# Optimization experiments

Hardware: AMD Instinct MI355X
Metric: run time of the kernel (lower is better)

Reference implementation:

```python
import jax, jax.numpy as jnp
import numpy as np

N_SRC = 100_000
N_DST = 100_000
N_EDGES = 1_600_000
D_IN = 256
N_HEADS = 4
OUT_FEATS = 32
NEG_SLOPE = 0.2


def setup_inputs() -> dict:
    key = jax.random.key(0)
    k1, k2, k3, k4, k5, k6, k7 = jax.random.split(key, 7)
    return {
        "feat_src": jax.random.normal(k1, (N_SRC, D_IN), dtype=jnp.float32),
        "feat_dst": jax.random.normal(k2, (N_DST, D_IN), dtype=jnp.float32),
        "w_src": jax.random.normal(k3, (D_IN, N_HEADS * OUT_FEATS), dtype=jnp.float32) * 0.05,
        "w_dst": jax.random.normal(k4, (D_IN, N_HEADS * OUT_FEATS), dtype=jnp.float32) * 0.05,
        "attn": jax.random.normal(k5, (N_HEADS, 2 * OUT_FEATS), dtype=jnp.float32) * 0.05,
        "src_idx": jax.random.randint(k6, (N_EDGES,), 0, N_SRC, dtype=jnp.int32),
        "dst_idx": jax.random.randint(k7, (N_EDGES,), 0, N_DST, dtype=jnp.int32),
    }


def reference(feat_src, feat_dst, w_src, w_dst, attn, src_idx, dst_idx):
    H, two_d = attn.shape
    D = two_d // 2
    n_dst = feat_dst.shape[0]
    # node transformations (dropout rate = 0.0 -> identity)
    fs = (feat_src @ w_src).reshape(-1, H, D)   # [Ns, H, D]
    fd = (feat_dst @ w_dst).reshape(-1, H, D)   # [Nd, H, D]
    # per-node attention logits: e_dst uses first half, e_src second half
    e_dst = (fd * attn[:, :D]).sum(-1)          # [Nd, H]
    e_src = (fs * attn[:, D:]).sum(-1)          # [Ns, H]
    # u_add_v on edges + leaky relu
    e = e_src[src_idx] + e_dst[dst_idx]         # [E, H]
    e = jnp.where(e > 0, e, NEG_SLOPE * e)
    # edge softmax: segment softmax over incoming edges of each dst node
    m = jax.ops.segment_max(e, dst_idx, num_segments=n_dst)       # [Nd, H]
    m = jnp.where(jnp.isfinite(m), m, 0.0)                        # empty segments
    ex = jnp.exp(e - m[dst_idx])                                  # [E, H]
    denom = jax.ops.segment_sum(ex, dst_idx, num_segments=n_dst)  # [Nd, H]
    a = ex / denom[dst_idx]                                       # [E, H]
    # u_mul_e + sum aggregation
    msg = fs[src_idx] * a[:, :, None]                             # [E, H, D]
    out = jax.ops.segment_sum(msg, dst_idx, num_segments=n_dst)   # [Nd, H, D]
    return jax.nn.relu(out.reshape(n_dst, H * D))
```

## Files before the change

### kernel.cpp

```cpp
#include <hip/hip_runtime.h>

#define N_NODES 100000
#define N_EDGES 1600000
#define D_IN    256
#define HD      128
#define NEG_SLOPE 0.2f

#define BUK_SH    5
#define BUK_NODES 32
#define NBUCKETS ((N_NODES + BUK_NODES - 1) / BUK_NODES)
#define BUK_CAP  1024
#define BUK_CH   8192
#define NB_BUK   ((N_EDGES + BUK_CH - 1) / BUK_CH)

#define NB_GEMM ((N_NODES + 255) / 256)
#define NB_EDST 256
#define NB_PREP 33

#define EX_STRIDE 1032

typedef __bf16 bf16x8 __attribute__((ext_vector_type(8)));
typedef float  f32x4  __attribute__((ext_vector_type(4)));

__device__ __forceinline__ float lrelu_exp(float v) {
  v = v > 0.f ? v : NEG_SLOPE * v;
  return __expf(v);
}
__device__ __forceinline__ float bf_lo(unsigned u) { return __uint_as_float(u << 16); }
__device__ __forceinline__ float bf_hi(unsigned u) { return __uint_as_float(u & 0xffff0000u); }

__global__ __launch_bounds__(1024) void prep_bucket_kernel(const float* __restrict__ w_src,
                                                           const float* __restrict__ w_dst,
                                                           const float* __restrict__ attn,
                                                           ushort* __restrict__ wT,
                                                           float* __restrict__ v_dst,
                                                           const int* __restrict__ src,
                                                           const int* __restrict__ dstv,
                                                           int* __restrict__ bcur,
                                                           unsigned* __restrict__ ebuk) {
  const int bid = blockIdx.x;
  const int tid = threadIdx.x;
  if (bid < 32) {
    int idx = bid * 1024 + tid;
    int k = idx >> 7, n = idx & 127;
    __bf16 bv = (__bf16)w_src[idx];
    wT[n * 256 + k] = *(const ushort*)&bv;
  } else if (bid == 32) {
    if (tid < 256) {
      int k = tid;
      for (int h = 0; h < 4; ++h) {
        float s = 0.f;
        for (int d = 0; d < 32; ++d)
          s += w_dst[k * HD + h * 32 + d] * attn[h * 64 + d];
        v_dst[k * 4 + h] = s;
      }
    }
  } else {
    __shared__ int bh[NBUCKETS];
    const int e0 = (bid - NB_PREP) * BUK_CH;
    for (int j = tid; j < NBUCKETS; j += 1024) bh[j] = 0;
    __syncthreads();
    for (int i = tid; i < BUK_CH; i += 1024) {
      int e = e0 + i;
      if (e < N_EDGES) atomicAdd(&bh[dstv[e] >> BUK_SH], 1);
    }
    __syncthreads();
    for (int j = tid; j < NBUCKETS; j += 1024) {
      int c = bh[j];
      bh[j] = (c > 0) ? atomicAdd(&bcur[j], c) : 0;
    }
    __syncthreads();
    for (int i = tid; i < BUK_CH; i += 1024) {
      int e = e0 + i;
      if (e < N_EDGES) {
        int d = dstv[e];
        int b = d >> BUK_SH;
        int p = atomicAdd(&bh[b], 1);
        if (p < BUK_CAP)
          ebuk[(size_t)b * BUK_CAP + p] =
              ((unsigned)src[e] << BUK_SH) | (unsigned)(d & (BUK_NODES - 1));
      }
    }
  }
}

__global__ __launch_bounds__(1024) void gemm_edst_kernel(const float* __restrict__ A,
                                                         const ushort* __restrict__ wT16,
                                                         const float* __restrict__ attn,
                                                         unsigned* __restrict__ fs16,
                                                         float* __restrict__ e_src,
                                                         const float* __restrict__ feat_dst,
                                                         const float* __restrict__ v_dst,
                                                         float* __restrict__ e_dst,
                                                         int M) {
  __shared__ ushort Bl[128 * 256];
  const int bid = blockIdx.x;
  const int tid = threadIdx.x;
  const int lane = tid & 63, wid = tid >> 6;
  const int lr = lane & 15, hi = lane >> 4;

  if (bid < NB_GEMM) {
    {
      const uint4* wg4 = (const uint4*)wT16;
#pragma unroll
      for (int i = 0; i < 4; ++i) {
        int c = i * 1024 + tid;
        int col = c >> 5;
        unsigned byte = ((unsigned)c * 16u) ^ (((unsigned)col & 31u) << 4);
        *(uint4*)((char*)Bl + byte) = wg4[c];
      }
    }

    f32x4 acc[8];
    const f32x4 zf = {0.f, 0.f, 0.f, 0.f};
#pragma unroll
    for (int n = 0; n < 8; ++n) acc[n] = zf;

    const int bm = bid * 256;
    int row0 = bm + wid * 16 + lr;
    int row0c = row0 < M ? row0 : M - 1;
    const float* a0p = A + (size_t)row0c * D_IN;

    __syncthreads();

#pragma unroll
    for (int ks = 0; ks < 8; ++ks) {
      const int ko = ks * 32 + hi * 8;
      float4 u0 = *(const float4*)(a0p + ko);
      float4 u1 = *(const float4*)(a0p + ko + 4);
      bf16x8 af0;
      af0[0] = (__bf16)u0.x; af0[1] = (__bf16)u0.y; af0[2] = (__bf16)u0.z; af0[3] = (__bf16)u0.w;
      af0[4] = (__bf16)u1.x; af0[5] = (__bf16)u1.y; af0[6] = (__bf16)u1.z; af0[7] = (__bf16)u1.w;
      bf16x8 bf[8];
#pragma unroll
      for (int n = 0; n < 8; ++n) {
        unsigned col = (unsigned)(n * 16 + lr);
        unsigned byte = (col * 512u + (unsigned)(ks * 64 + hi * 16)) ^ ((col & 31u) << 4);
        bf[n] = *(const bf16x8*)((const char*)Bl + byte);
      }
#pragma unroll
      for (int n = 0; n < 8; ++n)
        acc[n] = __builtin_amdgcn_mfma_f32_16x16x32_bf16(af0, bf[n], acc[n], 0, 0, 0);
    }

#pragma unroll
    for (int n = 0; n < 8; ++n) {
#pragma unroll
      for (int r4 = 0; r4 < 4; ++r4) {
        float val = acc[n][r4];
        float pv  = __shfl_xor(val, 1, 64);
        int gr = bm + wid * 16 + hi * 4 + r4;
        if (!(lane & 1) && gr < M) {
          __bf16 b0 = (__bf16)val, b1 = (__bf16)pv;
          unsigned pk = ((unsigned)*(const ushort*)&b1 << 16) | *(const ushort*)&b0;
          fs16[(size_t)gr * 64 + n * 8 + (lr >> 1)] = pk;
        }
      }
    }

#pragma unroll
    for (int gh = 0; gh < 4; ++gh) {
      float av0 = attn[gh * 64 + 32 + lr];
      float av1 = attn[gh * 64 + 48 + lr];
#pragma unroll
      for (int r4 = 0; r4 < 4; ++r4) {
        float s = acc[2 * gh][r4] * av0 + acc[2 * gh + 1][r4] * av1;
        s += __shfl_xor(s, 1, 64);
        s += __shfl_xor(s, 2, 64);
        s += __shfl_xor(s, 4, 64);
        s += __shfl_xor(s, 8, 64);
        int gr = bm + wid * 16 + hi * 4 + r4;
        if (lr == 0 && gr < M) e_src[(size_t)gr * 4 + gh] = s;
      }
    }
  } else {
    float4* vds = (float4*)Bl;
    if (tid < 256) vds[tid] = ((const float4*)v_dst)[tid];
    __syncthreads();
    const int l = tid & 15;
    const int grp = tid >> 4;
    for (int n = (bid - NB_GEMM) * 64 + grp; n < N_NODES; n += NB_EDST * 64) {
      const float* fp = feat_dst + (size_t)n * D_IN;
      float ax = 0.f, ay = 0.f, az = 0.f, aw = 0.f;
#pragma unroll
      for (int c = 0; c < 4; ++c) {
        const int k0 = c * 64 + l * 4;
        float4 f = *(const float4*)(fp + k0);
        float4 v0 = vds[k0 + 0], v1 = vds[k0 + 1], v2 = vds[k0 + 2], v3 = vds[k0 + 3];
        ax = fmaf(f.x, v0.x, fmaf(f.y, v1.x, fmaf(f.z, v2.x, fmaf(f.w, v3.x, ax))));
        ay = fmaf(f.x, v0.y, fmaf(f.y, v1.y, fmaf(f.z, v2.y, fmaf(f.w, v3.y, ay))));
        az = fmaf(f.x, v0.z, fmaf(f.y, v1.z, fmaf(f.z, v2.z, fmaf(f.w, v3.z, az))));
        aw = fmaf(f.x, v0.w, fmaf(f.y, v1.w, fmaf(f.z, v2.w, fmaf(f.w, v3.w, aw))));
      }
#pragma unroll
      for (int off = 1; off < 16; off <<= 1) {
        ax += __shfl_xor(ax, off, 64);
        ay += __shfl_xor(ay, off, 64);
        az += __shfl_xor(az, off, 64);
        aw += __shfl_xor(aw, off, 64);
      }
      if (l == 0) *(float4*)(e_dst + (size_t)n * 4) = make_float4(ax, ay, az, aw);
    }
  }
}

__global__ __launch_bounds__(256) void agg_kernel(const unsigned* __restrict__ ebuk,
                                                  const int* __restrict__ bcur,
                                                  const float4* __restrict__ e_src,
                                                  const float4* __restrict__ e_dst,
                                                  const unsigned* __restrict__ fs16,
                                                  float* __restrict__ out, int N) {
  __shared__ unsigned sorted_e[BUK_CAP];
  __shared__ float ex_s[4][EX_STRIDE];
  __shared__ int lcnt[BUK_NODES];
  __shared__ int lofs_s[BUK_NODES + 1];
  __shared__ int lcur[BUK_NODES];
  const int tid = threadIdx.x;
  const int wslot = tid >> 6;
  const int lane = tid & 63;
  const int lo = blockIdx.x * BUK_NODES;
  const size_t start = (size_t)blockIdx.x * BUK_CAP;
  const int cnt_e = min(bcur[blockIdx.x], BUK_CAP);

  if (tid < BUK_NODES) lcnt[tid] = 0;
  __syncthreads();
  for (int i = tid; i < cnt_e; i += 256)
    atomicAdd(&lcnt[ebuk[start + i] & (BUK_NODES - 1)], 1);
  __syncthreads();
  if (tid == 0) {
    int run = 0;
    for (int j = 0; j < BUK_NODES; ++j) {
      lofs_s[j] = run; lcur[j] = run; run += lcnt[j];
    }
    lofs_s[BUK_NODES] = run;
  }
  __syncthreads();
  for (int i = tid; i < cnt_e; i += 256) {
    unsigned e = ebuk[start + i];
    int p = atomicAdd(&lcur[e & (BUK_NODES - 1)], 1);
    sorted_e[p] = e;
  }
  __syncthreads();

  for (int i = tid; i < cnt_e; i += 256) {
    unsigned ent = sorted_e[i];
    int s  = (int)(ent >> BUK_SH);
    int dl = (int)(ent & (BUK_NODES - 1));
    float4 a  = e_src[s];
    float4 ed = e_dst[lo + dl];
    ex_s[0][i] = lrelu_exp(a.x + ed.x);
    ex_s[1][i] = lrelu_exp(a.y + ed.y);
    ex_s[2][i] = lrelu_exp(a.z + ed.z);
    ex_s[3][i] = lrelu_exp(a.w + ed.w);
  }
  __syncthreads();

  const int g = lane >> 4;
  const int q = lane & 15;
  const int h = q >> 2;

  for (int nl = wslot * 8; nl < wslot * 8 + 8; ++nl) {
    int node = lo + nl;
    if (node >= N) break;
    const int nb = lofs_s[nl], ne = lofs_s[nl + 1];
    float a0=0.f,a1=0.f,a2=0.f,a3=0.f,a4=0.f,a5=0.f,a6=0.f,a7=0.f,den=0.f;

    for (int cb = nb; cb < ne; cb += 16) {
      int e0 = cb + g, e1 = e0 + 4, e2 = e0 + 8, e3 = e0 + 12;
      bool p0 = e0 < ne, p1 = e1 < ne, p2 = e2 < ne, p3 = e3 < ne;
      int c0 = p0 ? e0 : nb, c1 = p1 ? e1 : nb, c2 = p2 ? e2 : nb, c3 = p3 ? e3 : nb;
      int s0 = (int)(sorted_e[c0] >> BUK_SH);
      int s1 = (int)(sorted_e[c1] >> BUK_SH);
      int s2 = (int)(sorted_e[c2] >> BUK_SH);
      int s3 = (int)(sorted_e[c3] >> BUK_SH);
      uint4 u0 = *(const uint4*)(fs16 + (size_t)s0 * 64 + q * 4);
      uint4 u1 = *(const uint4*)(fs16 + (size_t)s1 * 64 + q * 4);
      uint4 u2 = *(const uint4*)(fs16 + (size_t)s2 * 64 + q * 4);
      uint4 u3 = *(const uint4*)(fs16 + (size_t)s3 * 64 + q * 4);
      float x0 = p0 ? ex_s[h][c0] : 0.f;
      float x1 = p1 ? ex_s[h][c1] : 0.f;
      float x2 = p2 ? ex_s[h][c2] : 0.f;
      float x3 = p3 ? ex_s[h][c3] : 0.f;
      a0 = fmaf(x0, bf_lo(u0.x), a0); a1 = fmaf(x0, bf_hi(u0.x), a1);
      a2 = fmaf(x0, bf_lo(u0.y), a2); a3 = fmaf(x0, bf_hi(u0.y), a3);
      a4 = fmaf(x0, bf_lo(u0.z), a4); a5 = fmaf(x0, bf_hi(u0.z), a5);
      a6 = fmaf(x0, bf_lo(u0.w), a6); a7 = fmaf(x0, bf_hi(u0.w), a7);
      a0 = fmaf(x1, bf_lo(u1.x), a0); a1 = fmaf(x1, bf_hi(u1.x), a1);
      a2 = fmaf(x1, bf_lo(u1.y), a2); a3 = fmaf(x1, bf_hi(u1.y), a3);
      a4 = fmaf(x1, bf_lo(u1.z), a4); a5 = fmaf(x1, bf_hi(u1.z), a5);
      a6 = fmaf(x1, bf_lo(u1.w), a6); a7 = fmaf(x1, bf_hi(u1.w), a7);
      a0 = fmaf(x2, bf_lo(u2.x), a0); a1 = fmaf(x2, bf_hi(u2.x), a1);
      a2 = fmaf(x2, bf_lo(u2.y), a2); a3 = fmaf(x2, bf_hi(u2.y), a3);
      a4 = fmaf(x2, bf_lo(u2.z), a4); a5 = fmaf(x2, bf_hi(u2.z), a5);
      a6 = fmaf(x2, bf_lo(u2.w), a6); a7 = fmaf(x2, bf_hi(u2.w), a7);
      a0 = fmaf(x3, bf_lo(u3.x), a0); a1 = fmaf(x3, bf_hi(u3.x), a1);
      a2 = fmaf(x3, bf_lo(u3.y), a2); a3 = fmaf(x3, bf_hi(u3.y), a3);
      a4 = fmaf(x3, bf_lo(u3.z), a4); a5 = fmaf(x3, bf_hi(u3.z), a5);
      a6 = fmaf(x3, bf_lo(u3.w), a6); a7 = fmaf(x3, bf_hi(u3.w), a7);
      den += x0 + x1 + x2 + x3;
    }

    den += __shfl_xor(den, 16, 64); den += __shfl_xor(den, 32, 64);
    a0 += __shfl_xor(a0, 16, 64); a0 += __shfl_xor(a0, 32, 64);
    a1 += __shfl_xor(a1, 16, 64); a1 += __shfl_xor(a1, 32, 64);
    a2 += __shfl_xor(a2, 16, 64); a2 += __shfl_xor(a2, 32, 64);
    a3 += __shfl_xor(a3, 16, 64); a3 += __shfl_xor(a3, 32, 64);
    a4 += __shfl_xor(a4, 16, 64); a4 += __shfl_xor(a4, 32, 64);
    a5 += __shfl_xor(a5, 16, 64); a5 += __shfl_xor(a5, 32, 64);
    a6 += __shfl_xor(a6, 16, 64); a6 += __shfl_xor(a6, 32, 64);
    a7 += __shfl_xor(a7, 16, 64); a7 += __shfl_xor(a7, 32, 64);
    if (lane < 16) {
      float inv = den > 0.f ? 1.f / den : 0.f;
      float4 o1, o2;
      o1.x = fmaxf(a0 * inv, 0.f); o1.y = fmaxf(a1 * inv, 0.f);
      o1.z = fmaxf(a2 * inv, 0.f); o1.w = fmaxf(a3 * inv, 0.f);
      o2.x = fmaxf(a4 * inv, 0.f); o2.y = fmaxf(a5 * inv, 0.f);
      o2.z = fmaxf(a6 * inv, 0.f); o2.w = fmaxf(a7 * inv, 0.f);
      float* op = out + (size_t)node * HD + q * 8;
      *(float4*)(op)     = o1;
      *(float4*)(op + 4) = o2;
    }
  }
}

extern "C" void kernel_launch(void* const* d_in, const int* in_sizes, int n_in,
                              void* d_out, int out_size, void* d_ws, size_t ws_size,
                              hipStream_t stream) {
  const float* feat_src = (const float*)d_in[0];
  const float* feat_dst = (const float*)d_in[1];
  const float* w_src    = (const float*)d_in[2];
  const float* w_dst    = (const float*)d_in[3];
  const float* attn     = (const float*)d_in[4];
  const int*   src_idx  = (const int*)d_in[5];
  const int*   dst_idx  = (const int*)d_in[6];
  float* out = (float*)d_out;
  char* ws = (char*)d_ws;

  unsigned* fs16  = (unsigned*)(ws);
  float*    e_src = (float*)(ws + 25600000);
  float*    e_dst = (float*)(ws + 27200000);
  unsigned* ebuk  = (unsigned*)(ws + 28800000);
  float*    v_dst = (float*)(ws + 41600000);
  ushort*   wT16  = (ushort*)(ws + 41604096);
  int*      bcur  = (int*)  (ws + 41669632);

  hipMemsetAsync(bcur, 0, NBUCKETS * sizeof(int), stream);

  prep_bucket_kernel<<<NB_PREP + NB_BUK, 1024, 0, stream>>>(
      w_src, w_dst, attn, wT16, v_dst, src_idx, dst_idx, bcur, ebuk);

  gemm_edst_kernel<<<NB_GEMM + NB_EDST, 1024, 0, stream>>>(
      feat_src, wT16, attn, fs16, e_src, feat_dst, v_dst, e_dst, N_NODES);

  agg_kernel<<<NBUCKETS, 256, 0, stream>>>(ebuk, bcur,
      (const float4*)e_src, (const float4*)e_dst, fs16, out, N_NODES);
}
```

Baseline: 164.9 us.

## Split GEMM and e_dst into separate kernels with smaller blocks and prefetched A rows

Splits the fused GEMM/e_dst kernel into a dedicated MFMA GEMM kernel (512 threads, 128 rows per block, launch bounds allowing 4 blocks per CU) and a separate e_dst dot-product kernel (256 threads, 1024 blocks). The GEMM now issues all A-row global loads up front, before the barrier and the MFMA loop, so memory latency overlaps the weight staging. The goal is better occupancy and load balance than the mixed 1024-thread launch. The cost is an extra kernel launch and the two phases no longer running concurrently in one grid, plus more registers held by the 16 prefetched float4 values.

```diff
diff --git a/kernel.cpp b/kernel.cpp
--- a/kernel.cpp
+++ b/kernel.cpp
@@ -12,10 +12,11 @@
 #define BUK_CAP  1024
 #define BUK_CH   8192
 #define NB_BUK   ((N_EDGES + BUK_CH - 1) / BUK_CH)
-
-#define NB_GEMM ((N_NODES + 255) / 256)
-#define NB_EDST 256
 #define NB_PREP 33
+
+#define GEMM_ROWS 128
+#define NB_GEMM ((N_NODES + GEMM_ROWS - 1) / GEMM_ROWS)
+#define NB_EDST 1024
 
 #define EX_STRIDE 1032
 
@@ -84,123 +85,129 @@
   }
 }
 
-__global__ __launch_bounds__(1024) void gemm_edst_kernel(const float* __restrict__ A,
-                                                         const ushort* __restrict__ wT16,
-                                                         const float* __restrict__ attn,
-                                                         unsigned* __restrict__ fs16,
-                                                         float* __restrict__ e_src,
-                                                         const float* __restrict__ feat_dst,
-                                                         const float* __restrict__ v_dst,
-                                                         float* __restrict__ e_dst,
-                                                         int M) {
+__global__ __launch_bounds__(512, 4) void gemm_kernel(const float* __restrict__ A,
+                                                      const ushort* __restrict__ wT16,
+                                                      const float* __restrict__ attn,
+                                                      unsigned* __restrict__ fs16,
+                                                      float* __restrict__ e_src,
+                                                      int M) {
   __shared__ ushort Bl[128 * 256];
   const int bid = blockIdx.x;
   const int tid = threadIdx.x;
   const int lane = tid & 63, wid = tid >> 6;
   const int lr = lane & 15, hi = lane >> 4;
 
-  if (bid < NB_GEMM) {
-    {
-      const uint4* wg4 = (const uint4*)wT16;
-#pragma unroll
-      for (int i = 0; i < 4; ++i) {
-        int c = i * 1024 + tid;
-        int col = c >> 5;
-        unsigned byte = ((unsigned)c * 16u) ^ (((unsigned)col & 31u) << 4);
-        *(uint4*)((char*)Bl + byte) = wg4[c];
+  {
+    const uint4* wg4 = (const uint4*)wT16;
+#pragma unroll
+    for (int i = 0; i < 8; ++i) {
+      int c = i * 512 + tid;
+      int col = c >> 5;
+      unsigned byte = ((unsigned)c * 16u) ^ (((unsigned)col & 31u) << 4);
+      *(uint4*)((char*)Bl + byte) = wg4[c];
+    }
+  }
+
+  const int bm = bid * GEMM_ROWS;
+  int row0 = bm + wid * 16 + lr;
+  int row0c = row0 < M ? row0 : M - 1;
+  const float* a0p = A + (size_t)row0c * D_IN;
+
+  float4 u[16];
+#pragma unroll
+  for (int ks = 0; ks < 8; ++ks) {
+    const int ko = ks * 32 + hi * 8;
+    u[2 * ks]     = *(const float4*)(a0p + ko);
+    u[2 * ks + 1] = *(const float4*)(a0p + ko + 4);
+  }
+
+  f32x4 acc[8];
+  const f32x4 zf = {0.f, 0.f, 0.f, 0.f};
+#pragma unroll
+  for (int n = 0; n < 8; ++n) acc[n] = zf;
+
+  __syncthreads();
+
+#pragma unroll
+  for (int ks = 0; ks < 8; ++ks) {
+    float4 u0 = u[2 * ks], u1 = u[2 * ks + 1];
+    bf16x8 af0;
+    af0[0] = (__bf16)u0.x; af0[1] = (__bf16)u0.y; af0[2] = (__bf16)u0.z; af0[3] = (__bf16)u0.w;
+    af0[4] = (__bf16)u1.x; af0[5] = (__bf16)u1.y; af0[6] = (__bf16)u1.z; af0[7] = (__bf16)u1.w;
+    bf16x8 bf[8];
+#pragma unroll
+    for (int n = 0; n < 8; ++n) {
+      unsigned col = (unsigned)(n * 16 + lr);
+      unsigned byte = (col * 512u + (unsigned)(ks * 64 + hi * 16)) ^ ((col & 31u) << 4);
+      bf[n] = *(const bf16x8*)((const char*)Bl + byte);
+    }
+#pragma unroll
+    for (int n = 0; n < 8; ++n)
+      acc[n] = __builtin_amdgcn_mfma_f32_16x16x32_bf16(af0, bf[n], acc[n], 0, 0, 0);
+  }
+
+#pragma unroll
+  for (int n = 0; n < 8; ++n) {
+#pragma unroll
+    for (int r4 = 0; r4 < 4; ++r4) {
+      float val = acc[n][r4];
+      float pv  = __shfl_xor(val, 1, 64);
+      int gr = bm + wid * 16 + hi * 4 + r4;
+      if (!(lane & 1) && gr < M) {
+        __bf16 b0 = (__bf16)val, b1 = (__bf16)pv;
+        unsigned pk = ((unsigned)*(const ushort*)&b1 << 16) | *(const ushort*)&b0;
+        fs16[(size_t)gr * 64 + n * 8 + (lr >> 1)] = pk;
       }
     }
-
-    f32x4 acc[8];
-    const f32x4 zf = {0.f, 0.f, 0.f, 0.f};
-#pragma unroll
-    for (int n = 0; n < 8; ++n) acc[n] = zf;
-
-    const int bm = bid * 256;
-    int row0 = bm + wid * 16 + lr;
-    int row0c = row0 < M ? row0 : M - 1;
-    const float* a0p = A + (size_t)row0c * D_IN;
-
-    __syncthreads();
-
-#pragma unroll
-    for (int ks = 0; ks < 8; ++ks) {
-      const int ko = ks * 32 + hi * 8;
-      float4 u0 = *(const float4*)(a0p + ko);
-      float4 u1 = *(const float4*)(a0p + ko + 4);
-      bf16x8 af0;
-      af0[0] = (__bf16)u0.x; af0[1] = (__bf16)u0.y; af0[2] = (__bf16)u0.z; af0[3] = (__bf16)u0.w;
-      af0[4] = (__bf16)u1.x; af0[5] = (__bf16)u1.y; af0[6] = (__bf16)u1.z; af0[7] = (__bf16)u1.w;
-      bf16x8 bf[8];
-#pragma unroll
-      for (int n = 0; n < 8; ++n) {
-        unsigned col = (unsigned)(n * 16 + lr);
-        unsigned byte = (col * 512u + (unsigned)(ks * 64 + hi * 16)) ^ ((col & 31u) << 4);
-        bf[n] = *(const bf16x8*)((const char*)Bl + byte);
-      }
-#pragma unroll
-      for (int n = 0; n < 8; ++n)
-        acc[n] = __builtin_amdgcn_mfma_f32_16x16x32_bf16(af0, bf[n], acc[n], 0, 0, 0);
-    }
-
-#pragma unroll
-    for (int n = 0; n < 8; ++n) {
-#pragma unroll
-      for (int r4 = 0; r4 < 4; ++r4) {
-        float val = acc[n][r4];
-        float pv  = __shfl_xor(val, 1, 64);
-        int gr = bm + wid * 16 + hi * 4 + r4;
-        if (!(lane & 1) && gr < M) {
-          __bf16 b0 = (__bf16)val, b1 = (__bf16)pv;
-          unsigned pk = ((unsigned)*(const ushort*)&b1 << 16) | *(const ushort*)&b0;
-          fs16[(size_t)gr * 64 + n * 8 + (lr >> 1)] = pk;
-        }
-      }
-    }
-
-#pragma unroll
-    for (int gh = 0; gh < 4; ++gh) {
-      float av0 = attn[gh * 64 + 32 + lr];
-      float av1 = attn[gh * 64 + 48 + lr];
-#pragma unroll
-      for (int r4 = 0; r4 < 4; ++r4) {
-        float s = acc[2 * gh][r4] * av0 + acc[2 * gh + 1][r4] * av1;
-        s += __shfl_xor(s, 1, 64);
-        s += __shfl_xor(s, 2, 64);
-        s += __shfl_xor(s, 4, 64);
-        s += __shfl_xor(s, 8, 64);
-        int gr = bm + wid * 16 + hi * 4 + r4;
-        if (lr == 0 && gr < M) e_src[(size_t)gr * 4 + gh] = s;
-      }
-    }
-  } else {
-    float4* vds = (float4*)Bl;
-    if (tid < 256) vds[tid] = ((const float4*)v_dst)[tid];
-    __syncthreads();
-    const int l = tid & 15;
-    const int grp = tid >> 4;
-    for (int n = (bid - NB_GEMM) * 64 + grp; n < N_NODES; n += NB_EDST * 64) {
-      const float* fp = feat_dst + (size_t)n * D_IN;
-      float ax = 0.f, ay = 0.f, az = 0.f, aw = 0.f;
-#pragma unroll
-      for (int c = 0; c < 4; ++c) {
-        const int k0 = c * 64 + l * 4;
-        float4 f = *(const float4*)(fp + k0);
-        float4 v0 = vds[k0 + 0], v1 = vds[k0 + 1], v2 = vds[k0 + 2], v3 = vds[k0 + 3];
-        ax = fmaf(f.x, v0.x, fmaf(f.y, v1.x, fmaf(f.z, v2.x, fmaf(f.w, v3.x, ax))));
-        ay = fmaf(f.x, v0.y, fmaf(f.y, v1.y, fmaf(f.z, v2.y, fmaf(f.w, v3.y, ay))));
-        az = fmaf(f.x, v0.z, fmaf(f.y, v1.z, fmaf(f.z, v2.z, fmaf(f.w, v3.z, az))));
-        aw = fmaf(f.x, v0.w, fmaf(f.y, v1.w, fmaf(f.z, v2.w, fmaf(f.w, v3.w, aw))));
-      }
-#pragma unroll
-      for (int off = 1; off < 16; off <<= 1) {
-        ax += __shfl_xor(ax, off, 64);
-        ay += __shfl_xor(ay, off, 64);
-        az += __shfl_xor(az, off, 64);
-        aw += __shfl_xor(aw, off, 64);
-      }
-      if (l == 0) *(float4*)(e_dst + (size_t)n * 4) = make_float4(ax, ay, az, aw);
-    }
+  }
+
+#pragma unroll
+  for (int gh = 0; gh < 4; ++gh) {
+    float av0 = attn[gh * 64 + 32 + lr];
+    float av1 = attn[gh * 64 + 48 + lr];
+#pragma unroll
+    for (int r4 = 0; r4 < 4; ++r4) {
+      float s = acc[2 * gh][r4] * av0 + acc[2 * gh + 1][r4] * av1;
+      s += __shfl_xor(s, 1, 64);
+      s += __shfl_xor(s, 2, 64);
+      s += __shfl_xor(s, 4, 64);
+      s += __shfl_xor(s, 8, 64);
+      int gr = bm + wid * 16 + hi * 4 + r4;
+      if (lr == 0 && gr < M) e_src[(size_t)gr * 4 + gh] = s;
+    }
+  }
+}
+
+__global__ __launch_bounds__(256) void edst_kernel(const float* __restrict__ feat_dst,
+                                                   const float* __restrict__ v_dst,
+                                                   float* __restrict__ e_dst) {
+  __shared__ float4 vds[256];
+  const int tid = threadIdx.x;
+  vds[tid] = ((const float4*)v_dst)[tid];
+  __syncthreads();
+  const int l = tid & 15;
+  const int grp = tid >> 4;
+  for (int n = blockIdx.x * 16 + grp; n < N_NODES; n += NB_EDST * 16) {
+    const float* fp = feat_dst + (size_t)n * D_IN;
+    float ax = 0.f, ay = 0.f, az = 0.f, aw = 0.f;
+#pragma unroll
+    for (int c = 0; c < 4; ++c) {
+      const int k0 = c * 64 + l * 4;
+      float4 f = *(const float4*)(fp + k0);
+      float4 v0 = vds[k0 + 0], v1 = vds[k0 + 1], v2 = vds[k0 + 2], v3 = vds[k0 + 3];
+      ax = fmaf(f.x, v0.x, fmaf(f.y, v1.x, fmaf(f.z, v2.x, fmaf(f.w, v3.x, ax))));
+      ay = fmaf(f.x, v0.y, fmaf(f.y, v1.y, fmaf(f.z, v2.y, fmaf(f.w, v3.y, ay))));
+      az = fmaf(f.x, v0.z, fmaf(f.y, v1.z, fmaf(f.z, v2.z, fmaf(f.w, v3.z, az))));
+      aw = fmaf(f.x, v0.w, fmaf(f.y, v1.w, fmaf(f.z, v2.w, fmaf(f.w, v3.w, aw))));
+    }
+#pragma unroll
+    for (int off = 1; off < 16; off <<= 1) {
+      ax += __shfl_xor(ax, off, 64);
+      ay += __shfl_xor(ay, off, 64);
+      az += __shfl_xor(az, off, 64);
+      aw += __shfl_xor(aw, off, 64);
+    }
+    if (l == 0) *(float4*)(e_dst + (size_t)n * 4) = make_float4(ax, ay, az, aw);
   }
 }
 
@@ -349,8 +356,9 @@
   prep_bucket_kernel<<<NB_PREP + NB_BUK, 1024, 0, stream>>>(
       w_src, w_dst, attn, wT16, v_dst, src_idx, dst_idx, bcur, ebuk);
 
-  gemm_edst_kernel<<<NB_GEMM + NB_EDST, 1024, 0, stream>>>(
-      feat_src, wT16, attn, fs16, e_src, feat_dst, v_dst, e_dst, N_NODES);
+  gemm_kernel<<<NB_GEMM, 512, 0, stream>>>(feat_src, wT16, attn, fs16, e_src, N_NODES);
+
+  edst_kernel<<<NB_EDST, 256, 0, stream>>>(feat_dst, v_dst, e_dst);
 
   agg_kernel<<<NBUCKETS, 256, 0, stream>>>(ebuk, bcur,
       (const float4*)e_src, (const float4*)e_dst, fs16, out, N_NODES);
```

Result: slower. 176.5 us (+7.0%).
